# Kernel tuning notes

Hardware: AMD Instinct MI355X
Metric: run time of the kernel (lower is better)

The kernel has to match this reference:

```python
import jax, jax.numpy as jnp
import numpy as np
from jax import lax

BZ, CAP, SEQ, INV = 32, 134, 144, 16
E_SP, E_FT = 1072, 64


def sage(x, e_src, e_dst, Wl, bl, Wr, n_nodes):
    # PyG SAGEConv (mean aggr): out = lin_l(mean_{j->i} x_j) + lin_r(x_i)
    # x: [B, N, F]; edges broadcast over batch
    msgs = x[:, e_src]                                   # [B, E, F] gather
    agg = jnp.zeros_like(x).at[:, e_dst].add(msgs)        # [B, N, F] scatter-add
    deg = jnp.zeros((n_nodes,), x.dtype).at[e_dst].add(1.0)
    mean = agg / jnp.clip(deg, 1.0)[None, :, None]
    return mean @ Wl + bl + x @ Wr


def setup_inputs() -> dict:
    key = jax.random.key(0)
    ks = jax.random.split(key, 16)
    s = lambda fan: 1.0 / np.sqrt(fan)
    inp = {
        'src': jax.random.normal(ks[0], (BZ, CAP, SEQ, INV), jnp.float32),
        'graph_edge_index': jax.random.randint(ks[1], (2, E_SP), 0, CAP, jnp.int32),
        'feature_edge_index': jax.random.randint(ks[2], (2, E_FT), 0, INV, jnp.int32),
        # spatial SAGEConv(in_var, in_var)
        'gcn_Wl': jax.random.uniform(ks[3], (INV, INV), jnp.float32, -s(INV), s(INV)),
        'gcn_bl': jnp.zeros((INV,), jnp.float32),
        'gcn_Wr': jax.random.uniform(ks[4], (INV, INV), jnp.float32, -s(INV), s(INV)),
        # feature SAGEConv(seq_len, seq_len)
        'fgcn_Wl': jax.random.uniform(ks[5], (SEQ, SEQ), jnp.float32, -s(SEQ), s(SEQ)),
        'fgcn_bl': jnp.zeros((SEQ,), jnp.float32),
        'fgcn_Wr': jax.random.uniform(ks[6], (SEQ, SEQ), jnp.float32, -s(SEQ), s(SEQ)),
        # Conv1d(in_var, in_var, k=3/5, no bias): OIW layout
        'conv1_w': jax.random.uniform(ks[7], (INV, INV, 3), jnp.float32, -s(INV * 3), s(INV * 3)),
        'conv2_w': jax.random.uniform(ks[8], (INV, INV, 5), jnp.float32, -s(INV * 5), s(INV * 5)),
        # Linear(3*in_var, in_var)
        'fc_w': jax.random.uniform(ks[9], (3 * INV, INV), jnp.float32, -s(3 * INV), s(3 * INV)),
        'fc_b': jnp.zeros((INV,), jnp.float32),
    }
    return inp


def reference(src, graph_edge_index, feature_edge_index, gcn_Wl, gcn_bl, gcn_Wr,
              fgcn_Wl, fgcn_bl, fgcn_Wr, conv1_w, conv2_w, fc_w, fc_b):
    bz, cap, seq, inv = src.shape
    # --- spatial GCN: nodes = turbines, features = in_var, batched over bz*seq
    x1 = src.transpose(0, 2, 1, 3).reshape(bz * seq, cap, inv)
    sp = sage(x1, graph_edge_index[0], graph_edge_index[1], gcn_Wl, gcn_bl, gcn_Wr, cap)
    spatial_fea = sp.reshape(bz, seq, cap, inv).transpose(0, 2, 1, 3)
    # --- feature GCN: nodes = variables, features = seq_len, batched over bz*cap
    x2 = src.transpose(0, 1, 3, 2).reshape(bz * cap, inv, seq)
    ft = sage(x2, feature_edge_index[0], feature_edge_index[1], fgcn_Wl, fgcn_bl, fgcn_Wr, inv)
    fea_fea = ft.reshape(bz, cap, inv, seq).transpose(0, 1, 3, 2)
    # --- temporal dual Conv1d over seq axis, channels = in_var
    x3 = src.reshape(bz * cap, seq, inv).transpose(0, 2, 1)  # [N, C, L]
    dn = ('NCH', 'OIH', 'NCH')
    c1 = lax.conv_general_dilated(x3, conv1_w, (1,), [(1, 1)], dimension_numbers=dn)
    c2 = lax.conv_general_dilated(x3, conv2_w, (1,), [(2, 2)], dimension_numbers=dn)
    temporal_fea = (c1 + c2).transpose(0, 2, 1).reshape(bz, cap, seq, inv)
    # --- concat + FC fusion + residual (dropout = identity at eval)
    com = jnp.concatenate([spatial_fea, fea_fea, temporal_fea], axis=-1)  # [..., 3*inv]
    out = com @ fc_w + fc_b
    return src + out
```

## Files before the change

kernel.cpp:

```cpp
#include <hip/hip_runtime.h>
#include <hip/hip_bf16.h>

#define BZn 32
#define CAPn 134
#define SEQn 144
#define INVn 16
#define ESP 1072
#define EFT 64


typedef __attribute__((ext_vector_type(8))) short bf16x8;
typedef __attribute__((ext_vector_type(4))) short short4v;
typedef __attribute__((ext_vector_type(4))) float f32x4;

#define MFMA(a, b, c) __builtin_amdgcn_mfma_f32_16x16x32_bf16(a, b, c, 0, 0, 0)

__device__ __forceinline__ unsigned short f2bf(float f) {
    union { float f; unsigned u; } v; v.f = f;
    unsigned r = v.u + 0x7fff + ((v.u >> 16) & 1);
    return (unsigned short)(r >> 16);
}
__device__ __forceinline__ unsigned pk2(float a, float b) {
    float2 v; v.x = a; v.y = b;
    union { __hip_bfloat162 h; unsigned u; } c;
    c.h = __float22bfloat162_rn(v);
    return c.u;
}
__device__ __forceinline__ short4v pack4(f32x4 v) {
    union { unsigned u[2]; short4v s; } r;
    r.u[0] = pk2(v[0], v[1]);
    r.u[1] = pk2(v[2], v[3]);
    return r.s;
}

__global__ __launch_bounds__(256) void prep_kernel(
    const int* __restrict__ ge, const int* __restrict__ fe,
    const float* __restrict__ Wl,  const float* __restrict__ Wr,
    const float* __restrict__ fWl, const float* __restrict__ fWr,
    const float* __restrict__ w1,  const float* __restrict__ w2,
    const float* __restrict__ fcw,
    int* __restrict__ ws)
{
    int t = threadIdx.x;
    char* wsb = (char*)ws;
    unsigned short* ftB   = (unsigned short*)(wsb + 6144);
    unsigned short* featB = (unsigned short*)(wsb + 8192);
    unsigned short* convA = (unsigned short*)(wsb + 91136);
    unsigned short* spB   = (unsigned short*)(wsb + 95232);
    unsigned short* fcB   = (unsigned short*)(wsb + 96256);

    if (blockIdx.x == 0) {
        int* g_rp  = ws;
        int* g_col = ws + 135;
        float* g_inv = (float*)(ws + 1207);
        __shared__ int cnt[CAPn];
        __shared__ int off[CAPn];
        __shared__ int fm[256];
        __shared__ float finv[16];
        for (int c = t; c < CAPn; c += 256) cnt[c] = 0;
        fm[t] = 0;
        __syncthreads();
        for (int e = t; e < ESP; e += 256) atomicAdd(&cnt[ge[ESP + e]], 1);
        if (t < EFT) atomicAdd(&fm[fe[t] * 16 + fe[EFT + t]], 1);
        __syncthreads();
        if (t == 0) {
            int run = 0;
            for (int c = 0; c < CAPn; c++) {
                off[c] = run; g_rp[c] = run;
                g_inv[c] = 1.0f / fmaxf((float)cnt[c], 1.0f);
                run += cnt[c];
            }
            g_rp[CAPn] = run;
        }
        if (t < 16) {
            int dg = 0;
            for (int j = 0; j < 16; j++) dg += fm[j * 16 + t];
            finv[t] = 1.0f / fmaxf((float)dg, 1.0f);
        }
        __syncthreads();
        for (int c = t; c < CAPn; c += 256) cnt[c] = 0;
        __syncthreads();
        for (int e = t; e < ESP; e += 256) {
            int d = ge[ESP + e];
            int p = off[d] + atomicAdd(&cnt[d], 1);
            g_col[p] = ge[e];
        }
        for (int u = t; u < 512; u += 256) {
            int l = u >> 3, j = u & 7;
            int k = (l >> 4) * 8 + j, i = l & 15;
            float v = (k < 16) ? (float)fm[k * 16 + i] * finv[i] : 0.0f;
            ftB[u] = f2bf(v);
        }
    }

    int gt = blockIdx.x * 256 + t;
    int gs = gridDim.x * 256;
    for (int u = gt; u < 41472; u += gs) {
        int kk = u / 4608, rem = u - kk * 4608;
        int n0 = rem >> 9, rem2 = rem & 511;
        int l = rem2 >> 3, j = rem2 & 7;
        int k = kk * 32 + (l >> 4) * 8 + j;
        int s = n0 * 16 + (l & 15);
        float v = (k < 144) ? fWl[k * 144 + s] : fWr[(k - 144) * 144 + s];
        featB[u] = f2bf(v);
    }
    for (int u = gt; u < 2048; u += gs) {
        int kk = u >> 9, rem = u & 511;
        int l = rem >> 3, j = rem & 7;
        int q = l >> 4, o = l & 15;
        int kkp = kk * 2 + (q >> 1);
        int i = (q & 1) * 8 + j;
        float v = (kkp < 3) ? w1[(o * 16 + i) * 3 + kkp] : w2[(o * 16 + i) * 5 + (kkp - 3)];
        convA[u] = f2bf(v);
    }
    for (int u = gt; u < 512; u += gs) {
        int l = u >> 3, j = u & 7;
        int k = (l >> 4) * 8 + j, i = l & 15;
        float v = (k < 16) ? Wl[k * 16 + i] : Wr[(k - 16) * 16 + i];
        spB[u] = f2bf(v);
    }
    for (int u = gt; u < 1024; u += gs) {
        int kk = u >> 9, rem = u & 511;
        int l = rem >> 3, j = rem & 7;
        int k = kk * 32 + (l >> 4) * 8 + j, i = l & 15;
        float v = (k < 48) ? fcw[k * 16 + i] : 0.0f;
        fcB[u] = f2bf(v);
    }
}

__global__ __launch_bounds__(256, 3) void fused_kernel(
    const float* __restrict__ src,
    const float* __restrict__ bl,  const float* __restrict__ fbl,
    const float* __restrict__ fcb,
    const int* __restrict__ ws,
    float* __restrict__ out)
{
    const int* g_rp  = ws;
    const int* g_col = ws + 135;
    const float* g_inv = (const float*)(ws + 1207);
    const char* wsb = (const char*)ws;
    const unsigned short* ftB   = (const unsigned short*)(wsb + 6144);
    const unsigned short* featB = (const unsigned short*)(wsb + 8192);
    const unsigned short* convA = (const unsigned short*)(wsb + 91136);
    const unsigned short* spB   = (const unsigned short*)(wsb + 95232);
    const unsigned short* fcB   = (const unsigned short*)(wsb + 96256);

    __shared__ __align__(16) unsigned short xs_bf[SEQn + 4][24];
    __shared__ __align__(16) unsigned short xT_bf[INVn][152];
    __shared__ __align__(16) unsigned short meanft_bf[INVn][152];
    __shared__ __align__(16) unsigned short mean_sp_bf[SEQn][24];
    __shared__ __align__(16) unsigned short sp_bf[SEQn][24];
    __shared__ __align__(16) unsigned short ff_bf[SEQn][24];
    __shared__ __align__(16) unsigned short tp_bf[SEQn][24];
    __shared__ float sbl[16], sfcb[16], sfbl[SEQn];

    int t = threadIdx.x;
    int wave = t >> 6, lane = t & 63;
    int q = lane >> 4, ln = lane & 15;

    int xcd  = blockIdx.x & 7;
    int slot = blockIdx.x >> 3;
    int c  = slot >> 2;
    int b  = xcd * 4 + (slot & 3);
    int bc = b * CAPn + c;
    const float* srcb = src + (size_t)b * (CAPn * SEQn * INVn);
    const float* srcc = srcb + (size_t)c * (SEQn * INVn);

    bf16x8 caf[4];
    #pragma unroll
    for (int kk = 0; kk < 4; kk++)
        caf[kk] = *(const bf16x8*)(convA + (kk * 64 + lane) * 8);
    bf16x8 sbf  = *(const bf16x8*)(spB + lane * 8);
    bf16x8 ftf  = *(const bf16x8*)(ftB + lane * 8);
    bf16x8 fcf0 = *(const bf16x8*)(fcB + lane * 8);
    bf16x8 fcf1 = *(const bf16x8*)(fcB + (64 + lane) * 8);

    int rs = g_rp[c], re = g_rp[c + 1];
    float idg = g_inv[c];
    f32x4 m0 = {0.f,0.f,0.f,0.f}, m1 = {0.f,0.f,0.f,0.f}, m2 = {0.f,0.f,0.f,0.f};
    for (int e = rs; e < re; e++) {
        int n = g_col[e];
        const f32x4* p4 = (const f32x4*)(srcb + (size_t)n * (SEQn * INVn));
        m0 += p4[t];
        m1 += p4[t + 256];
        if (t < 64) m2 += p4[t + 512];
    }
    int s0g = t >> 2, i0g = (t & 3) * 4;
    m0 *= idg; m1 *= idg; m2 *= idg;
    *(short4v*)&mean_sp_bf[s0g][i0g]       = pack4(m0);
    *(short4v*)&mean_sp_bf[64 + s0g][i0g]  = pack4(m1);
    if (t < 64) *(short4v*)&mean_sp_bf[128 + s0g][i0g] = pack4(m2);

    const f32x4* s4 = (const f32x4*)srcc;
    f32x4 x0 = s4[t], x1 = s4[t + 256];
    short4v p0 = pack4(x0), p1 = pack4(x1);
    *(short4v*)&xs_bf[s0g + 2][i0g]      = p0;
    *(short4v*)&xs_bf[64 + s0g + 2][i0g] = p1;
    #pragma unroll
    for (int j = 0; j < 4; j++) {
        xT_bf[i0g + j][s0g]      = (unsigned short)p0[j];
        xT_bf[i0g + j][64 + s0g] = (unsigned short)p1[j];
    }
    if (t < 64) {
        f32x4 x2 = s4[t + 512];
        short4v p2 = pack4(x2);
        *(short4v*)&xs_bf[128 + s0g + 2][i0g] = p2;
        #pragma unroll
        for (int j = 0; j < 4; j++) xT_bf[i0g + j][128 + s0g] = (unsigned short)p2[j];
    }
    if (t < 64) {
        int r = t >> 4, i = t & 15;
        int row = (r < 2) ? r : 144 + r;
        xs_bf[row][i] = 0;
    }
    if (t < 16) { sbl[t] = bl[t]; sfcb[t] = fcb[t]; }
    if (t < SEQn) sfbl[t] = fbl[t];
    __syncthreads();

    const int mst[4] = {0, 0, 3, 6}, mcn[4] = {0, 3, 3, 3};
    const int cst[4] = {0, 3, 5, 7}, ccn[4] = {3, 2, 2, 2};
    const int sst[4] = {0, 2, 4, 6}, scn[4] = {2, 2, 2, 3};

    for (int tt = 0; tt < mcn[wave]; tt++) {
        int mt = mst[wave] + tt;
        int sl = mt * 16 + ln;
        bf16x8 a = {0,0,0,0,0,0,0,0};
        if (q < 2) a = *(const bf16x8*)&xs_bf[sl + 2][q * 8];
        f32x4 acc = {0.f,0.f,0.f,0.f};
        acc = MFMA(a, ftf, acc);
        *(short4v*)&meanft_bf[ln][mt * 16 + q * 4] = pack4(acc);
    }
    for (int tt = 0; tt < ccn[wave]; tt++) {
        int n0 = cst[wave] + tt;
        int sl = n0 * 16 + ln;
        f32x4 acc = {0.f,0.f,0.f,0.f};
        #pragma unroll
        for (int kk = 0; kk < 4; kk++) {
            int kkp = kk * 2 + (q >> 1);
            int off = (kkp < 3) ? (kkp - 1) : (kkp - 5);
            int i0 = (q & 1) * 8;
            bf16x8 bfr = *(const bf16x8*)&xs_bf[sl + 2 + off][i0];
            acc = MFMA(caf[kk], bfr, acc);
        }
        *(short4v*)&tp_bf[sl][q * 4] = pack4(acc);
    }
    for (int tt = 0; tt < scn[wave]; tt++) {
        int mt = sst[wave] + tt;
        int sl = mt * 16 + ln;
        const unsigned short* ap = (q < 2) ? &mean_sp_bf[sl][(q & 1) * 8]
                                           : &xs_bf[sl + 2][(q & 1) * 8];
        bf16x8 a = *(const bf16x8*)ap;
        f32x4 acc = {0.f,0.f,0.f,0.f};
        acc = MFMA(a, sbf, acc);
        #pragma unroll
        for (int r = 0; r < 4; r++)
            sp_bf[mt * 16 + q * 4 + r][ln] = f2bf(acc[r] + sbl[ln]);
    }
    __syncthreads();

    const int fst[4] = {0, 3, 5, 7}, fcn[4] = {3, 2, 2, 2};
    for (int tt = 0; tt < fcn[wave]; tt++) {
        int n0 = fst[wave] + tt;
        int sl = n0 * 16 + ln;
        f32x4 acc = {0.f,0.f,0.f,0.f};
        #pragma unroll
        for (int kk = 0; kk < 9; kk++) {
            int koff = kk * 32 + q * 8;
            const unsigned short* ap = (koff < 144) ? &meanft_bf[ln][koff]
                                                    : &xT_bf[ln][koff - 144];
            bf16x8 a = *(const bf16x8*)ap;
            bf16x8 bfr = *(const bf16x8*)(featB + ((kk * 9 + n0) * 64 + lane) * 8);
            acc = MFMA(a, bfr, acc);
        }
        *(short4v*)&ff_bf[sl][q * 4] = pack4(acc + sfbl[sl]);
    }
    __syncthreads();

    const int xst[4] = {0, 2, 4, 6}, xcn[4] = {2, 2, 2, 3};
    float* outb = out + (size_t)bc * (SEQn * INVn);
    for (int tt = 0; tt < xcn[wave]; tt++) {
        int mt = xst[wave] + tt;
        int sl = mt * 16 + ln;
        f32x4 acc = {0.f,0.f,0.f,0.f};
        {
            const unsigned short* ap = (q < 2) ? &sp_bf[sl][(q & 1) * 8]
                                               : &ff_bf[sl][(q & 1) * 8];
            bf16x8 a = *(const bf16x8*)ap;
            acc = MFMA(a, fcf0, acc);
        }
        {
            bf16x8 a = {0,0,0,0,0,0,0,0};
            if (q < 2) a = *(const bf16x8*)&tp_bf[sl][q * 8];
            acc = MFMA(a, fcf1, acc);
        }
        #pragma unroll
        for (int r = 0; r < 4; r++) {
            int so = mt * 16 + q * 4 + r;
            int idx = so * 16 + ln;
            outb[idx] = acc[r] + sfcb[ln] + srcc[idx];
        }
    }
}

extern "C" void kernel_launch(void* const* d_in, const int* in_sizes, int n_in,
                              void* d_out, int out_size, void* d_ws, size_t ws_size,
                              hipStream_t stream)
{
    const float* src = (const float*)d_in[0];
    const int* ge = (const int*)d_in[1];
    const int* fe = (const int*)d_in[2];
    const float* Wl  = (const float*)d_in[3];
    const float* blp = (const float*)d_in[4];
    const float* Wr  = (const float*)d_in[5];
    const float* fWl = (const float*)d_in[6];
    const float* fbl = (const float*)d_in[7];
    const float* fWr = (const float*)d_in[8];
    const float* w1  = (const float*)d_in[9];
    const float* w2  = (const float*)d_in[10];
    const float* fcw = (const float*)d_in[11];
    const float* fcb = (const float*)d_in[12];
    float* out = (float*)d_out;
    int* ws = (int*)d_ws;

    hipLaunchKernelGGL(prep_kernel, dim3(16), dim3(256), 0, stream,
                       ge, fe, Wl, Wr, fWl, fWr, w1, w2, fcw, ws);
    hipLaunchKernelGGL(fused_kernel, dim3(BZn * CAPn), dim3(256), 0, stream,
                       src, blp, fbl, fcb, ws, out);
}
```

Measured before the change: 175.4 us.

## Fold final FC weights into spatial, feature and conv weights to cut intermediates

Precomputes the products of the FC weights with the spatial SAGE, feature-graph and conv weights in the prep kernel. The fused kernel can then skip the separate FC stage and the transposed copy of x. Conv and feature-GCN contributions accumulate into one MFMA accumulator, spatial results stay in registers, and biases fold into a per-channel constant plus a sequence-dependent term. This cuts LDS buffers and passes, and raises the launch-bounds occupancy hint from 3 to 5. It also remaps blocks to batch/node and loads fW tiles through LDS in prep. Folding the weights changes where bf16 rounding happens, which may shift numerical error.

```diff
diff --git a/kernel.cpp b/kernel.cpp
--- a/kernel.cpp
+++ b/kernel.cpp
@@ -20,6 +20,10 @@
     unsigned r = v.u + 0x7fff + ((v.u >> 16) & 1);
     return (unsigned short)(r >> 16);
 }
+__device__ __forceinline__ float bf2f(unsigned short h) {
+    union { unsigned u; float f; } v; v.u = ((unsigned)h) << 16;
+    return v.f;
+}
 __device__ __forceinline__ unsigned pk2(float a, float b) {
     float2 v; v.x = a; v.y = b;
     union { __hip_bfloat162 h; unsigned u; } c;
@@ -38,26 +42,28 @@
     const float* __restrict__ Wl,  const float* __restrict__ Wr,
     const float* __restrict__ fWl, const float* __restrict__ fWr,
     const float* __restrict__ w1,  const float* __restrict__ w2,
-    const float* __restrict__ fcw,
+    const float* __restrict__ fcw, const float* __restrict__ bl,
+    const float* __restrict__ fcb,
     int* __restrict__ ws)
 {
     int t = threadIdx.x;
     char* wsb = (char*)ws;
-    unsigned short* ftB   = (unsigned short*)(wsb + 6144);
-    unsigned short* featB = (unsigned short*)(wsb + 8192);
-    unsigned short* convA = (unsigned short*)(wsb + 91136);
-    unsigned short* spB   = (unsigned short*)(wsb + 95232);
-    unsigned short* fcB   = (unsigned short*)(wsb + 96256);
+    unsigned short* uB     = (unsigned short*)(wsb + 5376);
+    unsigned short* vB     = (unsigned short*)(wsb + 6400);
+    unsigned short* spB2   = (unsigned short*)(wsb + 7424);
+    float*          biasf  = (float*)(wsb + 8448);
+    unsigned short* convA2 = (unsigned short*)(wsb + 8704);
+    unsigned short* featB  = (unsigned short*)(wsb + 12800);
+
+    __shared__ float wtile[32][145];
 
     if (blockIdx.x == 0) {
         int* g_rp  = ws;
         int* g_col = ws + 135;
         float* g_inv = (float*)(ws + 1207);
-        __shared__ int cnt[CAPn];
-        __shared__ int off[CAPn];
-        __shared__ int fm[256];
+        __shared__ int cnt[CAPn], off[CAPn], fm[256];
         __shared__ float finv[16];
-        for (int c = t; c < CAPn; c += 256) cnt[c] = 0;
+        for (int c0 = t; c0 < CAPn; c0 += 256) cnt[c0] = 0;
         fm[t] = 0;
         __syncthreads();
         for (int e = t; e < ESP; e += 256) atomicAdd(&cnt[ge[ESP + e]], 1);
@@ -65,10 +71,10 @@
         __syncthreads();
         if (t == 0) {
             int run = 0;
-            for (int c = 0; c < CAPn; c++) {
-                off[c] = run; g_rp[c] = run;
-                g_inv[c] = 1.0f / fmaxf((float)cnt[c], 1.0f);
-                run += cnt[c];
+            for (int c0 = 0; c0 < CAPn; c0++) {
+                off[c0] = run; g_rp[c0] = run;
+                g_inv[c0] = 1.0f / fmaxf((float)cnt[c0], 1.0f);
+                run += cnt[c0];
             }
             g_rp[CAPn] = run;
         }
@@ -78,7 +84,7 @@
             finv[t] = 1.0f / fmaxf((float)dg, 1.0f);
         }
         __syncthreads();
-        for (int c = t; c < CAPn; c += 256) cnt[c] = 0;
+        for (int c0 = t; c0 < CAPn; c0 += 256) cnt[c0] = 0;
         __syncthreads();
         for (int e = t; e < ESP; e += 256) {
             int d = ge[ESP + e];
@@ -86,52 +92,56 @@
             g_col[p] = ge[e];
         }
         for (int u = t; u < 512; u += 256) {
-            int l = u >> 3, j = u & 7;
-            int k = (l >> 4) * 8 + j, i = l & 15;
-            float v = (k < 16) ? (float)fm[k * 16 + i] * finv[i] : 0.0f;
-            ftB[u] = f2bf(v);
-        }
-    }
-
-    int gt = blockIdx.x * 256 + t;
-    int gs = gridDim.x * 256;
-    for (int u = gt; u < 41472; u += gs) {
-        int kk = u / 4608, rem = u - kk * 4608;
-        int n0 = rem >> 9, rem2 = rem & 511;
-        int l = rem2 >> 3, j = rem2 & 7;
-        int k = kk * 32 + (l >> 4) * 8 + j;
-        int s = n0 * 16 + (l & 15);
-        float v = (k < 144) ? fWl[k * 144 + s] : fWr[(k - 144) * 144 + s];
-        featB[u] = f2bf(v);
-    }
-    for (int u = gt; u < 2048; u += gs) {
-        int kk = u >> 9, rem = u & 511;
+            int l = u >> 3, j = u & 7, k = (l >> 4) * 8 + j, ip = l & 15;
+            float vu = 0.f, vv = 0.f, vs = 0.f;
+            if (k < 16) {
+                for (int i = 0; i < 16; i++)
+                    vu += (float)fm[k * 16 + i] * finv[i] * fcw[(16 + i) * 16 + ip];
+                vv = fcw[(16 + k) * 16 + ip];
+                for (int i = 0; i < 16; i++) vs += Wl[k * 16 + i] * fcw[i * 16 + ip];
+            } else {
+                for (int i = 0; i < 16; i++) vs += Wr[(k - 16) * 16 + i] * fcw[i * 16 + ip];
+            }
+            uB[u] = f2bf(vu); vB[u] = f2bf(vv); spB2[u] = f2bf(vs);
+        }
+        for (int u = t; u < 2048; u += 256) {
+            int kk2 = u >> 9, l = (u >> 3) & 63, j = u & 7, q = l >> 4, o = l & 15;
+            int kkp = kk2 * 2 + (q >> 1), i = (q & 1) * 8 + j;
+            float v = 0.f;
+            for (int o0 = 0; o0 < 16; o0++) {
+                float w = (kkp < 3) ? w1[(o0 * 16 + i) * 3 + kkp]
+                                    : w2[(o0 * 16 + i) * 5 + (kkp - 3)];
+                v += w * fcw[(32 + o0) * 16 + o];
+            }
+            convA2[u] = f2bf(v);
+        }
+        if (t < 16) {
+            float b0 = fcb[t], c0 = 0.f;
+            for (int i = 0; i < 16; i++) {
+                b0 += bl[i] * fcw[i * 16 + t];
+                c0 += fcw[(16 + i) * 16 + t];
+            }
+            biasf[t] = b0; biasf[16 + t] = c0;
+        }
+    }
+
+    int kk = blockIdx.x;
+    for (int u = t; u < 32 * 144; u += 256) {
+        int r = u / 144, s = u - r * 144;
+        int k = kk * 32 + r;
+        wtile[r][s] = (k < 144) ? fWl[k * 144 + s] : fWr[(k - 144) * 144 + s];
+    }
+    __syncthreads();
+    for (int u = t; u < 4608; u += 256) {
+        int n0 = u >> 9, rem = u & 511;
         int l = rem >> 3, j = rem & 7;
-        int q = l >> 4, o = l & 15;
-        int kkp = kk * 2 + (q >> 1);
-        int i = (q & 1) * 8 + j;
-        float v = (kkp < 3) ? w1[(o * 16 + i) * 3 + kkp] : w2[(o * 16 + i) * 5 + (kkp - 3)];
-        convA[u] = f2bf(v);
-    }
-    for (int u = gt; u < 512; u += gs) {
-        int l = u >> 3, j = u & 7;
-        int k = (l >> 4) * 8 + j, i = l & 15;
-        float v = (k < 16) ? Wl[k * 16 + i] : Wr[(k - 16) * 16 + i];
-        spB[u] = f2bf(v);
-    }
-    for (int u = gt; u < 1024; u += gs) {
-        int kk = u >> 9, rem = u & 511;
-        int l = rem >> 3, j = rem & 7;
-        int k = kk * 32 + (l >> 4) * 8 + j, i = l & 15;
-        float v = (k < 48) ? fcw[k * 16 + i] : 0.0f;
-        fcB[u] = f2bf(v);
-    }
-}
-
-__global__ __launch_bounds__(256, 3) void fused_kernel(
+        featB[(kk * 9 + n0) * 512 + rem] = f2bf(wtile[(l >> 4) * 8 + j][n0 * 16 + (l & 15)]);
+    }
+}
+
+__global__ __launch_bounds__(256, 5) void fused_kernel(
     const float* __restrict__ src,
-    const float* __restrict__ bl,  const float* __restrict__ fbl,
-    const float* __restrict__ fcb,
+    const float* __restrict__ fbl,
     const int* __restrict__ ws,
     float* __restrict__ out)
 {
@@ -139,20 +149,18 @@
     const int* g_col = ws + 135;
     const float* g_inv = (const float*)(ws + 1207);
     const char* wsb = (const char*)ws;
-    const unsigned short* ftB   = (const unsigned short*)(wsb + 6144);
-    const unsigned short* featB = (const unsigned short*)(wsb + 8192);
-    const unsigned short* convA = (const unsigned short*)(wsb + 91136);
-    const unsigned short* spB   = (const unsigned short*)(wsb + 95232);
-    const unsigned short* fcB   = (const unsigned short*)(wsb + 96256);
+    const unsigned short* uB     = (const unsigned short*)(wsb + 5376);
+    const unsigned short* vB     = (const unsigned short*)(wsb + 6400);
+    const unsigned short* spB2   = (const unsigned short*)(wsb + 7424);
+    const float*          biasf  = (const float*)(wsb + 8448);
+    const unsigned short* convA2 = (const unsigned short*)(wsb + 8704);
+    const unsigned short* featB  = (const unsigned short*)(wsb + 12800);
 
     __shared__ __align__(16) unsigned short xs_bf[SEQn + 4][24];
-    __shared__ __align__(16) unsigned short xT_bf[INVn][152];
-    __shared__ __align__(16) unsigned short meanft_bf[INVn][152];
-    __shared__ __align__(16) unsigned short mean_sp_bf[SEQn][24];
-    __shared__ __align__(16) unsigned short sp_bf[SEQn][24];
-    __shared__ __align__(16) unsigned short ff_bf[SEQn][24];
-    __shared__ __align__(16) unsigned short tp_bf[SEQn][24];
-    __shared__ float sbl[16], sfcb[16], sfbl[SEQn];
+    __shared__ __align__(16) unsigned short msp_bf[SEQn][24];
+    __shared__ __align__(16) unsigned short uv_bf[INVn][312];
+    __shared__ __align__(16) unsigned short t_bf[SEQn][24];
+    __shared__ float sfbl[SEQn], sbias[16], scs[16];
 
     int t = threadIdx.x;
     int wave = t >> 6, lane = t & 63;
@@ -160,20 +168,20 @@
 
     int xcd  = blockIdx.x & 7;
     int slot = blockIdx.x >> 3;
-    int c  = slot >> 2;
-    int b  = xcd * 4 + (slot & 3);
-    int bc = b * CAPn + c;
+    int bl_  = slot / 134;
+    int c    = slot - bl_ * 134;
+    int b    = xcd * 4 + bl_;
+    int bc   = b * CAPn + c;
     const float* srcb = src + (size_t)b * (CAPn * SEQn * INVn);
     const float* srcc = srcb + (size_t)c * (SEQn * INVn);
 
     bf16x8 caf[4];
     #pragma unroll
     for (int kk = 0; kk < 4; kk++)
-        caf[kk] = *(const bf16x8*)(convA + (kk * 64 + lane) * 8);
-    bf16x8 sbf  = *(const bf16x8*)(spB + lane * 8);
-    bf16x8 ftf  = *(const bf16x8*)(ftB + lane * 8);
-    bf16x8 fcf0 = *(const bf16x8*)(fcB + lane * 8);
-    bf16x8 fcf1 = *(const bf16x8*)(fcB + (64 + lane) * 8);
+        caf[kk] = *(const bf16x8*)(convA2 + (kk * 64 + lane) * 8);
+    bf16x8 sbf = *(const bf16x8*)(spB2 + lane * 8);
+    bf16x8 ubf = *(const bf16x8*)(uB + lane * 8);
+    bf16x8 vbf = *(const bf16x8*)(vB + lane * 8);
 
     int rs = g_rp[c], re = g_rp[c + 1];
     float idg = g_inv[c];
@@ -187,117 +195,83 @@
     }
     int s0g = t >> 2, i0g = (t & 3) * 4;
     m0 *= idg; m1 *= idg; m2 *= idg;
-    *(short4v*)&mean_sp_bf[s0g][i0g]       = pack4(m0);
-    *(short4v*)&mean_sp_bf[64 + s0g][i0g]  = pack4(m1);
-    if (t < 64) *(short4v*)&mean_sp_bf[128 + s0g][i0g] = pack4(m2);
+    *(short4v*)&msp_bf[s0g][i0g]      = pack4(m0);
+    *(short4v*)&msp_bf[64 + s0g][i0g] = pack4(m1);
+    if (t < 64) *(short4v*)&msp_bf[128 + s0g][i0g] = pack4(m2);
 
     const f32x4* s4 = (const f32x4*)srcc;
     f32x4 x0 = s4[t], x1 = s4[t + 256];
-    short4v p0 = pack4(x0), p1 = pack4(x1);
-    *(short4v*)&xs_bf[s0g + 2][i0g]      = p0;
-    *(short4v*)&xs_bf[64 + s0g + 2][i0g] = p1;
-    #pragma unroll
-    for (int j = 0; j < 4; j++) {
-        xT_bf[i0g + j][s0g]      = (unsigned short)p0[j];
-        xT_bf[i0g + j][64 + s0g] = (unsigned short)p1[j];
-    }
+    *(short4v*)&xs_bf[s0g + 2][i0g]      = pack4(x0);
+    *(short4v*)&xs_bf[64 + s0g + 2][i0g] = pack4(x1);
     if (t < 64) {
         f32x4 x2 = s4[t + 512];
-        short4v p2 = pack4(x2);
-        *(short4v*)&xs_bf[128 + s0g + 2][i0g] = p2;
-        #pragma unroll
-        for (int j = 0; j < 4; j++) xT_bf[i0g + j][128 + s0g] = (unsigned short)p2[j];
+        *(short4v*)&xs_bf[128 + s0g + 2][i0g] = pack4(x2);
     }
     if (t < 64) {
         int r = t >> 4, i = t & 15;
         int row = (r < 2) ? r : 144 + r;
         xs_bf[row][i] = 0;
     }
-    if (t < 16) { sbl[t] = bl[t]; sfcb[t] = fcb[t]; }
     if (t < SEQn) sfbl[t] = fbl[t];
+    if (t < 16) { sbias[t] = biasf[t]; scs[t] = biasf[16 + t]; }
     __syncthreads();
 
-    const int mst[4] = {0, 0, 3, 6}, mcn[4] = {0, 3, 3, 3};
-    const int cst[4] = {0, 3, 5, 7}, ccn[4] = {3, 2, 2, 2};
-    const int sst[4] = {0, 2, 4, 6}, scn[4] = {2, 2, 2, 3};
-
-    for (int tt = 0; tt < mcn[wave]; tt++) {
-        int mt = mst[wave] + tt;
+    const int ust[4] = {0, 3, 5, 7}, ucn[4] = {3, 2, 2, 2};
+    for (int tt = 0; tt < ucn[wave]; tt++) {
+        int mt = ust[wave] + tt;
         int sl = mt * 16 + ln;
         bf16x8 a = {0,0,0,0,0,0,0,0};
         if (q < 2) a = *(const bf16x8*)&xs_bf[sl + 2][q * 8];
-        f32x4 acc = {0.f,0.f,0.f,0.f};
-        acc = MFMA(a, ftf, acc);
-        *(short4v*)&meanft_bf[ln][mt * 16 + q * 4] = pack4(acc);
-    }
-    for (int tt = 0; tt < ccn[wave]; tt++) {
-        int n0 = cst[wave] + tt;
+        f32x4 au = {0.f,0.f,0.f,0.f}, av = {0.f,0.f,0.f,0.f};
+        au = MFMA(a, ubf, au);
+        av = MFMA(a, vbf, av);
+        *(short4v*)&uv_bf[ln][mt * 16 + q * 4]       = pack4(au);
+        *(short4v*)&uv_bf[ln][144 + mt * 16 + q * 4] = pack4(av);
+    }
+    const int sst[4] = {0, 2, 4, 6}, scn[4] = {2, 2, 2, 3};
+    f32x4 accS[3];
+    for (int tt = 0; tt < scn[wave]; tt++) {
+        int mt = sst[wave] + tt;
+        int sl = mt * 16 + ln;
+        const unsigned short* ap = (q < 2) ? &msp_bf[sl][(q & 1) * 8]
+                                           : &xs_bf[sl + 2][(q & 1) * 8];
+        bf16x8 a = *(const bf16x8*)ap;
+        f32x4 z = {0.f,0.f,0.f,0.f};
+        accS[tt] = MFMA(a, sbf, z);
+    }
+    __syncthreads();
+
+    const int bst[4] = {0, 3, 5, 7}, bcn[4] = {3, 2, 2, 2};
+    for (int tt = 0; tt < bcn[wave]; tt++) {
+        int n0 = bst[wave] + tt;
         int sl = n0 * 16 + ln;
         f32x4 acc = {0.f,0.f,0.f,0.f};
         #pragma unroll
         for (int kk = 0; kk < 4; kk++) {
             int kkp = kk * 2 + (q >> 1);
             int off = (kkp < 3) ? (kkp - 1) : (kkp - 5);
-            int i0 = (q & 1) * 8;
-            bf16x8 bfr = *(const bf16x8*)&xs_bf[sl + 2 + off][i0];
-            acc = MFMA(caf[kk], bfr, acc);
-        }
-        *(short4v*)&tp_bf[sl][q * 4] = pack4(acc);
-    }
+            bf16x8 bb = *(const bf16x8*)&xs_bf[sl + 2 + off][(q & 1) * 8];
+            acc = MFMA(caf[kk], bb, acc);
+        }
+        #pragma unroll
+        for (int kk = 0; kk < 9; kk++) {
+            bf16x8 a  = *(const bf16x8*)&uv_bf[ln][kk * 32 + q * 8];
+            bf16x8 bb = *(const bf16x8*)(featB + ((kk * 9 + n0) * 64 + lane) * 8);
+            acc = MFMA(a, bb, acc);
+        }
+        *(short4v*)&t_bf[sl][q * 4] = pack4(acc);
+    }
+    __syncthreads();
+
+    float* outb = out + (size_t)bc * (SEQn * INVn);
     for (int tt = 0; tt < scn[wave]; tt++) {
         int mt = sst[wave] + tt;
-        int sl = mt * 16 + ln;
-        const unsigned short* ap = (q < 2) ? &mean_sp_bf[sl][(q & 1) * 8]
-                                           : &xs_bf[sl + 2][(q & 1) * 8];
-        bf16x8 a = *(const bf16x8*)ap;
-        f32x4 acc = {0.f,0.f,0.f,0.f};
-        acc = MFMA(a, sbf, acc);
-        #pragma unroll
-        for (int r = 0; r < 4; r++)
-            sp_bf[mt * 16 + q * 4 + r][ln] = f2bf(acc[r] + sbl[ln]);
-    }
-    __syncthreads();
-
-    const int fst[4] = {0, 3, 5, 7}, fcn[4] = {3, 2, 2, 2};
-    for (int tt = 0; tt < fcn[wave]; tt++) {
-        int n0 = fst[wave] + tt;
-        int sl = n0 * 16 + ln;
-        f32x4 acc = {0.f,0.f,0.f,0.f};
-        #pragma unroll
-        for (int kk = 0; kk < 9; kk++) {
-            int koff = kk * 32 + q * 8;
-            const unsigned short* ap = (koff < 144) ? &meanft_bf[ln][koff]
-                                                    : &xT_bf[ln][koff - 144];
-            bf16x8 a = *(const bf16x8*)ap;
-            bf16x8 bfr = *(const bf16x8*)(featB + ((kk * 9 + n0) * 64 + lane) * 8);
-            acc = MFMA(a, bfr, acc);
-        }
-        *(short4v*)&ff_bf[sl][q * 4] = pack4(acc + sfbl[sl]);
-    }
-    __syncthreads();
-
-    const int xst[4] = {0, 2, 4, 6}, xcn[4] = {2, 2, 2, 3};
-    float* outb = out + (size_t)bc * (SEQn * INVn);
-    for (int tt = 0; tt < xcn[wave]; tt++) {
-        int mt = xst[wave] + tt;
-        int sl = mt * 16 + ln;
-        f32x4 acc = {0.f,0.f,0.f,0.f};
-        {
-            const unsigned short* ap = (q < 2) ? &sp_bf[sl][(q & 1) * 8]
-                                               : &ff_bf[sl][(q & 1) * 8];
-            bf16x8 a = *(const bf16x8*)ap;
-            acc = MFMA(a, fcf0, acc);
-        }
-        {
-            bf16x8 a = {0,0,0,0,0,0,0,0};
-            if (q < 2) a = *(const bf16x8*)&tp_bf[sl][q * 8];
-            acc = MFMA(a, fcf1, acc);
-        }
         #pragma unroll
         for (int r = 0; r < 4; r++) {
-            int so = mt * 16 + q * 4 + r;
-            int idx = so * 16 + ln;
-            outb[idx] = acc[r] + sfcb[ln] + srcc[idx];
+            int s = mt * 16 + q * 4 + r;
+            int idx = s * 16 + ln;
+            outb[idx] = accS[tt][r] + bf2f(t_bf[s][ln]) + srcc[idx]
+                      + sbias[ln] + sfbl[s] * scs[ln];
         }
     }
 }
@@ -322,8 +296,8 @@
     float* out = (float*)d_out;
     int* ws = (int*)d_ws;
 
-    hipLaunchKernelGGL(prep_kernel, dim3(16), dim3(256), 0, stream,
-                       ge, fe, Wl, Wr, fWl, fWr, w1, w2, fcw, ws);
+    hipLaunchKernelGGL(prep_kernel, dim3(9), dim3(256), 0, stream,
+                       ge, fe, Wl, Wr, fWl, fWr, w1, w2, fcw, blp, fcb, ws);
     hipLaunchKernelGGL(fused_kernel, dim3(BZn * CAPn), dim3(256), 0, stream,
-                       src, blp, fbl, fcb, ws, out);
-}
+                       src, fbl, ws, out);
+}
```

Result: faster. 171.6 us (-2.1%).
